# Optimization experiments

Hardware: AMD Instinct MI355X
Metric: run time of the kernel (lower is better)

Reference implementation:

```python
import jax, jax.numpy as jnp
import numpy as np

H = 56; W = 56; WS = 7; NW = WS * WS  # 49 tokens per window
HEADS = 8; DIM = 256; HIDDEN = 4 * DIM
SHIFT = NW // 2  # gilbert shift = 24 (shift_size > 0)
SCALE = (DIM // HEADS) ** -0.5
EPS = 1e-5


def _sgn(v):
    return -1 if v < 0 else 1 if v > 0 else 0


def _generate2d(x, y, ax, ay, bx, by, result):
    w = abs(ax + ay); h = abs(bx + by)
    dax, day = _sgn(ax), _sgn(ay); dbx, dby = _sgn(bx), _sgn(by)
    if h == 1 or w == 1:
        if h == 1:
            for _ in range(w):
                result.append((x, y)); x, y = x + dax, y + day
        elif w == 1:
            for _ in range(h):
                result.append((x, y)); x, y = x + dbx, y + dby
        return
    ax2, ay2 = ax // 2, ay // 2; bx2, by2 = bx // 2, by // 2
    w2 = abs(ax2 + ay2); h2 = abs(bx2 + by2)
    if 2 * w > 3 * h:
        if w2 % 2 and w > 2:
            ax2, ay2 = ax2 + dax, ay2 + day
        _generate2d(x, y, ax2, ay2, bx, by, result)
        _generate2d(x + ax2, y + ay2, ax - ax2, ay - ay2, bx, by, result)
    else:
        if h2 % 2 and h > 2:
            bx2, by2 = bx2 + dbx, by2 + dby
        _generate2d(x, y, bx2, by2, ax2, ay2, result)
        _generate2d(x + bx2, y + by2, ax, ay, bx - bx2, by - by2, result)
        _generate2d(x + (ax - dax) + (bx2 - dbx), y + (ay - day) + (by2 - dby),
                    -bx2, -by2, -(ax - ax2), -(ay - ay2), result)


def _gilbert2d(width, height):
    result = []
    if width >= height:
        _generate2d(0, 0, width, 0, 0, height, result)
    else:
        _generate2d(0, 0, 0, height, width, 0, result)
    return result


def _make_rel_index():
    # reverse_map[idx] = (y, x) for gilbert position idx
    path = _gilbert2d(W, H)
    rev = np.zeros((H * W, 2), dtype=np.int64)
    for i, (px, py) in enumerate(path[:H * W]):
        rev[i, 0] = py; rev[i, 1] = px
    pos = np.roll(rev, SHIFT, axis=0)  # shifted block: roll positions by ws^2//2
    n_windows = (H * W) // NW
    pos = pos[:n_windows * NW].reshape(n_windows, NW, 2)
    dh = pos[:, :, 0][:, :, None] - pos[:, :, 0][:, None, :] + (H - 1)
    dw = pos[:, :, 1][:, :, None] - pos[:, :, 1][:, None, :] + (W - 1)
    return (dh * (2 * W - 1) + dw).astype(np.int32)  # (nW, 49, 49)


def setup_inputs() -> dict:
    key = jax.random.key(0)
    ks = jax.random.split(key, 8)
    B, L, C = 32, H * W, DIM
    return {
        "x": jax.random.normal(ks[0], (B, L, C), jnp.float32),
        "qkv_w": jax.random.normal(ks[1], (C, 3 * C), jnp.float32) * 0.02,
        "qkv_b": jnp.zeros((3 * C,), jnp.float32),
        "proj_w": jax.random.normal(ks[2], (C, C), jnp.float32) * 0.02,
        "proj_b": jnp.zeros((C,), jnp.float32),
        "bias_table": jax.random.normal(ks[3], ((2 * H - 1) * (2 * W - 1), HEADS), jnp.float32) * 0.02,
        "norm1_w": jnp.ones((C,), jnp.float32),
        "norm1_b": jnp.zeros((C,), jnp.float32),
        "norm2_w": jnp.ones((C,), jnp.float32),
        "norm2_b": jnp.zeros((C,), jnp.float32),
        "fc1_w": jax.random.normal(ks[4], (C, HIDDEN), jnp.float32) * 0.02,
        "fc1_b": jnp.zeros((HIDDEN,), jnp.float32),
        "fc2_w": jax.random.normal(ks[5], (HIDDEN, C), jnp.float32) * 0.02,
        "fc2_b": jnp.zeros((C,), jnp.float32),
        "rel_index": jnp.asarray(_make_rel_index()),
    }


def _layernorm(x, w, b):
    mu = jnp.mean(x, axis=-1, keepdims=True)
    var = jnp.mean(jnp.square(x - mu), axis=-1, keepdims=True)
    return (x - mu) * jax.lax.rsqrt(var + EPS) * w + b


def reference(x, qkv_w, qkv_b, proj_w, proj_b, bias_table,
              norm1_w, norm1_b, norm2_w, norm2_b,
              fc1_w, fc1_b, fc2_w, fc2_b, rel_index):
    B, L, C = x.shape
    n_win = L // NW
    hd = C // HEADS

    shortcut = x
    h = _layernorm(x, norm1_w, norm1_b)
    # gilbert forward shift along the curve, then window partition
    h = jnp.roll(h, SHIFT, axis=1)
    hw = h.reshape(B * n_win, NW, C)

    qkv = (hw @ qkv_w + qkv_b).reshape(B * n_win, NW, 3, HEADS, hd)
    qkv = jnp.transpose(qkv, (2, 0, 3, 1, 4))  # (3, B*nW, heads, N, hd)
    q, k, v = qkv[0] * SCALE, qkv[1], qkv[2]

    attn = jnp.einsum('bhnd,bhmd->bhnm', q, k)  # (B*nW, heads, 49, 49)
    bias = jnp.transpose(bias_table[rel_index], (0, 3, 1, 2))  # (nW, heads, 49, 49)
    attn = attn.reshape(B, n_win, HEADS, NW, NW) + bias[None]
    attn = jax.nn.softmax(attn, axis=-1).reshape(B * n_win, HEADS, NW, NW)

    out = jnp.einsum('bhnm,bhmd->bhnd', attn, v)
    out = jnp.transpose(out, (0, 2, 1, 3)).reshape(B * n_win, NW, C)
    out = out @ proj_w + proj_b

    # window merge + gilbert reverse shift
    out = out.reshape(B, L, C)
    out = jnp.roll(out, -SHIFT, axis=1)

    x = shortcut + out
    h2 = _layernorm(x, norm2_w, norm2_b)
    h2 = jax.nn.gelu(h2 @ fc1_w + fc1_b, approximate=False) @ fc2_w + fc2_b
    return x + h2
```

## Files before the change

kernel.cpp:

```cpp
#include <hip/hip_runtime.h>
#include <math.h>

typedef unsigned short u16;
typedef __attribute__((ext_vector_type(8))) short bfrag;
typedef __attribute__((ext_vector_type(4))) float f32x4;
typedef __attribute__((ext_vector_type(4))) unsigned short us4;

#define B_SZ 32
#define L_SZ 3136
#define C_SZ 256
#define NHEADS 8
#define HID_SZ 1024
#define NW 49
#define NWIN 64
#define SHIFT 24
#define M_SZ (B_SZ * L_SZ)
#define SCALEF 0.17677669529663687f

__device__ __forceinline__ float bf2f(u16 u) {
  union { unsigned int i; float f; } v; v.i = ((unsigned)u) << 16; return v.f;
}
__device__ __forceinline__ u16 f2bf(float f) {
  union { unsigned int i; float f; } v; v.f = f;
  return (u16)((v.i + 0x7fffu + ((v.i >> 16) & 1u)) >> 16);
}
__device__ __forceinline__ void gload_lds16(const u16* g, u16* l) {
  __builtin_amdgcn_global_load_lds(
      (const __attribute__((address_space(1))) unsigned int*)g,
      (__attribute__((address_space(3))) unsigned int*)l, 16, 0, 0);
}

__global__ void transpose_kernel(const float* __restrict__ in, u16* __restrict__ out,
                                 int K, int N) {
  const int idx = blockIdx.x * 256 + threadIdx.x;
  if (idx >= K * N) return;
  const int n = idx / K;
  const int k = idx - n * K;
  out[idx] = f2bf(in[(size_t)k * N + n]);
}

__global__ void bias_kernel(const float* __restrict__ tab, const int* __restrict__ rel,
                            float* __restrict__ bm) {
  const int idx = blockIdx.x * 256 + threadIdx.x;
  const int tot = NWIN * NHEADS * NW * NW;
  if (idx >= tot) return;
  const int w = idx / (NHEADS * NW * NW);
  const int r = idx - w * (NHEADS * NW * NW);
  const int h = r / (NW * NW);
  const int ij = r - h * (NW * NW);
  bm[idx] = tab[(size_t)rel[w * NW * NW + ij] * NHEADS + h];
}

__global__ __launch_bounds__(256) void ln1_kernel(
    const float* __restrict__ x, const float* __restrict__ w,
    const float* __restrict__ b, u16* __restrict__ out) {
  const int wv = threadIdx.x >> 6;
  const int lane = threadIdx.x & 63;
  const int row0 = blockIdx.x * 16 + wv * 4;
  float4 u[4];
#pragma unroll
  for (int r = 0; r < 4; ++r)
    u[r] = *((const float4*)x + (size_t)(row0 + r) * 64 + lane);
  float s[4], sq[4];
#pragma unroll
  for (int r = 0; r < 4; ++r) {
    s[r]  = u[r].x + u[r].y + u[r].z + u[r].w;
    sq[r] = u[r].x * u[r].x + u[r].y * u[r].y + u[r].z * u[r].z + u[r].w * u[r].w;
  }
#pragma unroll
  for (int d = 1; d < 64; d <<= 1)
#pragma unroll
    for (int r = 0; r < 4; ++r) {
      s[r] += __shfl_xor(s[r], d); sq[r] += __shfl_xor(sq[r], d);
    }
  float wv4[4], bv4[4];
#pragma unroll
  for (int j = 0; j < 4; ++j) { wv4[j] = w[lane * 4 + j]; bv4[j] = b[lane * 4 + j]; }
#pragma unroll
  for (int r = 0; r < 4; ++r) {
    const int row = row0 + r;
    const float mu = s[r] * (1.0f / C_SZ);
    const float rs = rsqrtf(sq[r] * (1.0f / C_SZ) - mu * mu + 1e-5f);
    const int bb = row / L_SZ;
    int l2 = row - bb * L_SZ + SHIFT;
    if (l2 >= L_SZ) l2 -= L_SZ;
    const float vv[4] = {u[r].x, u[r].y, u[r].z, u[r].w};
    us4 ov;
#pragma unroll
    for (int j = 0; j < 4; ++j) ov[j] = f2bf((vv[j] - mu) * rs * wv4[j] + bv4[j]);
    *(us4*)(out + ((size_t)bb * L_SZ + l2) * C_SZ + lane * 4) = ov;
  }
}

__global__ __launch_bounds__(256) void ln2_kernel(
    const u16* __restrict__ x, const float* __restrict__ w,
    const float* __restrict__ b, u16* __restrict__ out) {
  const int wv = threadIdx.x >> 6;
  const int lane = threadIdx.x & 63;
  const int row0 = blockIdx.x * 16 + wv * 4;
  us4 u[4];
#pragma unroll
  for (int r = 0; r < 4; ++r)
    u[r] = *(const us4*)(x + (size_t)(row0 + r) * C_SZ + lane * 4);
  float v[4][4], s[4], sq[4];
#pragma unroll
  for (int r = 0; r < 4; ++r) {
    s[r] = 0.f; sq[r] = 0.f;
#pragma unroll
    for (int j = 0; j < 4; ++j) {
      v[r][j] = bf2f(u[r][j]); s[r] += v[r][j]; sq[r] += v[r][j] * v[r][j];
    }
  }
#pragma unroll
  for (int d = 1; d < 64; d <<= 1)
#pragma unroll
    for (int r = 0; r < 4; ++r) {
      s[r] += __shfl_xor(s[r], d); sq[r] += __shfl_xor(sq[r], d);
    }
  float wv4[4], bv4[4];
#pragma unroll
  for (int j = 0; j < 4; ++j) { wv4[j] = w[lane * 4 + j]; bv4[j] = b[lane * 4 + j]; }
#pragma unroll
  for (int r = 0; r < 4; ++r) {
    const float mu = s[r] * (1.0f / C_SZ);
    const float rs = rsqrtf(sq[r] * (1.0f / C_SZ) - mu * mu + 1e-5f);
    us4 ov;
#pragma unroll
    for (int j = 0; j < 4; ++j) ov[j] = f2bf((v[r][j] - mu) * rs * wv4[j] + bv4[j]);
    *(us4*)(out + (size_t)(row0 + r) * C_SZ + lane * 4) = ov;
  }
}

#define BM 128
#define BN 128
#define BKT 64

template <int MODE>
__global__ __launch_bounds__(256, 2) void gemm_kernel(
    const u16* __restrict__ A, const u16* __restrict__ Bt,
    const float* __restrict__ bias, int N, int K, void* __restrict__ Cout,
    const float* __restrict__ resx, u16* __restrict__ vt,
    const u16* __restrict__ resb2) {
  __shared__ u16 Als[BM * BKT];
  __shared__ u16 Bls[BN * BKT];
  const int tid = threadIdx.x;
  const int lane = tid & 63;
  const int lr = lane & 15;
  const int lg = lane >> 4;
  const int m0 = blockIdx.y * BM;
  const int n0 = blockIdx.x * BN;
  const int wid = tid >> 6;
  const int wm = (wid >> 1) * 64;
  const int wn = (wid & 1) * 64;

  const int grow = lane >> 3;
  const int gch = (lane & 7) ^ grow;

  const f32x4 fzero = {0.f, 0.f, 0.f, 0.f};
  f32x4 acc[4][4];
#pragma unroll
  for (int i = 0; i < 4; ++i)
#pragma unroll
    for (int j = 0; j < 4; ++j) acc[i][j] = fzero;

  const u16* Agl = A + (size_t)m0 * K + gch * 8;
  const u16* Bgl = Bt + (size_t)n0 * K + gch * 8;

  for (int k0 = 0; k0 < K; k0 += BKT) {
#pragma unroll
    for (int g = 0; g < 4; ++g) {
      const int rbase = wid * 32 + g * 8;
      gload_lds16(Agl + (size_t)(rbase + grow) * K + k0, Als + rbase * 64);
      gload_lds16(Bgl + (size_t)(rbase + grow) * K + k0, Bls + rbase * 64);
    }
    __syncthreads();
#pragma unroll
    for (int s = 0; s < 2; ++s) {
      const int kg = s * 4 + lg;
      bfrag af[4], bfv[4];
#pragma unroll
      for (int m = 0; m < 4; ++m) {
        const int r = wm + m * 16 + lr;
        af[m] = *(const bfrag*)(Als + r * 64 + ((kg ^ (r & 7)) * 8));
      }
#pragma unroll
      for (int n = 0; n < 4; ++n) {
        const int r = wn + n * 16 + lr;
        bfv[n] = *(const bfrag*)(Bls + r * 64 + ((kg ^ (r & 7)) * 8));
      }
#pragma unroll
      for (int m = 0; m < 4; ++m)
#pragma unroll
        for (int n = 0; n < 4; ++n)
          acc[m][n] = __builtin_amdgcn_mfma_f32_16x16x32_bf16(af[m], bfv[n],
                                                              acc[m][n], 0, 0, 0);
    }
    __syncthreads();
  }

  float bv4[4];
#pragma unroll
  for (int n = 0; n < 4; ++n) bv4[n] = bias[n0 + wn + n * 16 + lr];

#pragma unroll
  for (int m = 0; m < 4; ++m) {
#pragma unroll
    for (int i = 0; i < 4; ++i) {
      const int row = m0 + wm + m * 16 + lg * 4 + i;
      if (MODE == 1) {
        const int bb = row / L_SZ;
        int l2 = row - bb * L_SZ - SHIFT;
        if (l2 < 0) l2 += L_SZ;
        const size_t orow = (size_t)bb * L_SZ + l2;
#pragma unroll
        for (int n = 0; n < 4; ++n) {
          const int col = n0 + wn + n * 16 + lr;
          ((u16*)Cout)[orow * N + col] =
              f2bf(resx[orow * N + col] + acc[m][n][i] + bv4[n]);
        }
      } else if (MODE == 2) {
#pragma unroll
        for (int n = 0; n < 4; ++n) {
          const int col = n0 + wn + n * 16 + lr;
          float v = acc[m][n][i] + bv4[n];
          v = 0.5f * v * (1.0f + erff(v * 0.70710678f));
          ((u16*)Cout)[(size_t)row * N + col] = f2bf(v);
        }
      } else if (MODE == 3) {
#pragma unroll
        for (int n = 0; n < 4; ++n) {
          const int col = n0 + wn + n * 16 + lr;
          ((float*)Cout)[(size_t)row * N + col] =
              acc[m][n][i] + bv4[n] + bf2f(resb2[(size_t)row * N + col]);
        }
      } else {
        if (n0 + wn < 512) {
#pragma unroll
          for (int n = 0; n < 4; ++n) {
            const int col = n0 + wn + n * 16 + lr;
            ((u16*)Cout)[(size_t)row * 512 + col] = f2bf(acc[m][n][i] + bv4[n]);
          }
        } else {
          const unsigned widx = (unsigned)row / 49u;
          const int kk = row - (int)widx * 49;
#pragma unroll
          for (int n = 0; n < 4; ++n) {
            const int col = n0 + wn + n * 16 + lr - 512;
            const int hh = col >> 5;
            const int d = col & 31;
            vt[(((size_t)widx * NHEADS + hh) * 32 + d) * 64 + kk] =
                f2bf(acc[m][n][i] + bv4[n]);
          }
        }
      }
    }
  }
}

__global__ __launch_bounds__(256) void attn_kernel(const u16* __restrict__ qk,
                                                   const u16* __restrict__ vt,
                                                   const float* __restrict__ bm,
                                                   u16* __restrict__ out) {
  __shared__ u16 Pls[4][64 * 72];
  const int widx = blockIdx.x >> 1;
  const int half = blockIdx.x & 1;
  const int w = widx & (NWIN - 1);
  const int wv = threadIdx.x >> 6;
  const int lane = threadIdx.x & 63;
  const int lr = lane & 15;
  const int lg = lane >> 4;
  const size_t base = (size_t)widx * NW;
  u16* P = Pls[wv];
  const f32x4 fzero = {0.f, 0.f, 0.f, 0.f};
  const int h = half * 4 + wv;

  bfrag qf[4], kf[4];
#pragma unroll
  for (int m = 0; m < 4; ++m) {
    int r = m * 16 + lr; if (r > NW - 1) r = NW - 1;
    qf[m] = *(const bfrag*)(qk + (base + r) * 512 + h * 32 + lg * 8);
    kf[m] = *(const bfrag*)(qk + (base + r) * 512 + 256 + h * 32 + lg * 8);
  }
  f32x4 s[4][4];
#pragma unroll
  for (int m = 0; m < 4; ++m)
#pragma unroll
    for (int n = 0; n < 4; ++n)
      s[m][n] = __builtin_amdgcn_mfma_f32_16x16x32_bf16(qf[m], kf[n], fzero, 0, 0, 0);

  const float* bh = bm + (size_t)(w * NHEADS + h) * (NW * NW);
#pragma unroll
  for (int m = 0; m < 4; ++m) {
#pragma unroll
    for (int i = 0; i < 4; ++i) {
      const int row = m * 16 + lg * 4 + i;
      const int brow = row > NW - 1 ? NW - 1 : row;
      float vals[4];
#pragma unroll
      for (int n = 0; n < 4; ++n) {
        const int c = n * 16 + lr;
        vals[n] = (c < NW) ? (s[m][n][i] * SCALEF + bh[brow * NW + c]) : -1e30f;
      }
      float mx = fmaxf(fmaxf(vals[0], vals[1]), fmaxf(vals[2], vals[3]));
#pragma unroll
      for (int d = 1; d < 16; d <<= 1) mx = fmaxf(mx, __shfl_xor(mx, d));
      float sum = 0.f;
#pragma unroll
      for (int n = 0; n < 4; ++n) { vals[n] = __expf(vals[n] - mx); sum += vals[n]; }
#pragma unroll
      for (int d = 1; d < 16; d <<= 1) sum += __shfl_xor(sum, d);
      const float inv = 1.0f / sum;
#pragma unroll
      for (int n = 0; n < 4; ++n)
        P[row * 72 + n * 16 + lr] = f2bf(vals[n] * inv);
    }
  }
  const u16* vth = vt + ((size_t)widx * NHEADS + h) * 32 * 64;
  f32x4 o[4][2];
#pragma unroll
  for (int m = 0; m < 4; ++m) { o[m][0] = fzero; o[m][1] = fzero; }
#pragma unroll
  for (int s2 = 0; s2 < 2; ++s2) {
    bfrag pf[4], vf[2];
#pragma unroll
    for (int m = 0; m < 4; ++m)
      pf[m] = *(const bfrag*)(P + (m * 16 + lr) * 72 + s2 * 32 + lg * 8);
#pragma unroll
    for (int n = 0; n < 2; ++n)
      vf[n] = *(const bfrag*)(vth + (size_t)(n * 16 + lr) * 64 + s2 * 32 + lg * 8);
#pragma unroll
    for (int m = 0; m < 4; ++m)
#pragma unroll
      for (int n = 0; n < 2; ++n)
        o[m][n] = __builtin_amdgcn_mfma_f32_16x16x32_bf16(pf[m], vf[n],
                                                          o[m][n], 0, 0, 0);
  }
#pragma unroll
  for (int m = 0; m < 4; ++m)
#pragma unroll
    for (int i = 0; i < 4; ++i) {
      const int row = m * 16 + lg * 4 + i;
      if (row < NW) {
#pragma unroll
        for (int n = 0; n < 2; ++n)
          out[(base + row) * C_SZ + h * 32 + n * 16 + lr] = f2bf(o[m][n][i]);
      }
    }
}

extern "C" void kernel_launch(void* const* d_in, const int* in_sizes, int n_in,
                              void* d_out, int out_size, void* d_ws, size_t ws_size,
                              hipStream_t stream) {
  (void)in_sizes; (void)n_in; (void)out_size;
  const float* x     = (const float*)d_in[0];
  const float* qkvw  = (const float*)d_in[1];
  const float* qkvb  = (const float*)d_in[2];
  const float* projw = (const float*)d_in[3];
  const float* projb = (const float*)d_in[4];
  const float* btab  = (const float*)d_in[5];
  const float* n1w   = (const float*)d_in[6];
  const float* n1b   = (const float*)d_in[7];
  const float* n2w   = (const float*)d_in[8];
  const float* n2b   = (const float*)d_in[9];
  const float* fc1w  = (const float*)d_in[10];
  const float* fc1b  = (const float*)d_in[11];
  const float* fc2w  = (const float*)d_in[12];
  const float* fc2b  = (const float*)d_in[13];
  const int* rel     = (const int*)d_in[14];

  char* ws = (char*)d_ws;
  size_t off = 0;
  auto alloc = [&](size_t bytes) -> char* {
    char* p = ws + off; off += (bytes + 255) & ~(size_t)255; return p;
  };
  u16* qkvwT   = (u16*)alloc((size_t)768 * 256 * 2);
  u16* projwT  = (u16*)alloc((size_t)256 * 256 * 2);
  u16* fc1wT   = (u16*)alloc((size_t)1024 * 256 * 2);
  u16* fc2wT   = (u16*)alloc((size_t)256 * 1024 * 2);
  float* biasm = (float*)alloc((size_t)NWIN * NHEADS * NW * NW * 4);
  u16* bufh    = (u16*)alloc((size_t)M_SZ * C_SZ * 2);
  u16* x2b     = (u16*)alloc((size_t)M_SZ * C_SZ * 2);

  char* tail = ws + off;
  u16* qkbuf = (u16*)tail;
  const size_t qk_bytes = (size_t)M_SZ * 512 * 2;
  u16* vtbuf = (u16*)(tail + qk_bytes);
  const size_t tail_attn = qk_bytes + (size_t)B_SZ * NWIN * NHEADS * 32 * 64 * 2;
  u16* scratch2 = (u16*)tail;
  const size_t full_scr = (size_t)M_SZ * HID_SZ * 2;
  const size_t tail_need1 = full_scr > tail_attn ? full_scr : tail_attn;
  const int nch = (ws_size >= off + tail_need1) ? 1 : 4;
  const int mch = M_SZ / nch;

  transpose_kernel<<<(256 * 768 + 255) / 256, 256, 0, stream>>>(qkvw, qkvwT, 256, 768);
  transpose_kernel<<<(256 * 256 + 255) / 256, 256, 0, stream>>>(projw, projwT, 256, 256);
  transpose_kernel<<<(256 * 1024 + 255) / 256, 256, 0, stream>>>(fc1w, fc1wT, 256, 1024);
  transpose_kernel<<<(1024 * 256 + 255) / 256, 256, 0, stream>>>(fc2w, fc2wT, 1024, 256);
  bias_kernel<<<(NWIN * NHEADS * NW * NW + 255) / 256, 256, 0, stream>>>(btab, rel, biasm);

  ln1_kernel<<<M_SZ / 16, 256, 0, stream>>>(x, n1w, n1b, bufh);

  gemm_kernel<0><<<dim3(768 / BN, M_SZ / BM), 256, 0, stream>>>(
      bufh, qkvwT, qkvb, 768, 256, qkbuf, nullptr, vtbuf, nullptr);

  attn_kernel<<<B_SZ * NWIN * 2, 256, 0, stream>>>(qkbuf, vtbuf, biasm, bufh);

  gemm_kernel<1><<<dim3(256 / BN, M_SZ / BM), 256, 0, stream>>>(
      bufh, projwT, projb, 256, 256, x2b, x, nullptr, nullptr);

  for (int q = 0; q < nch; ++q) {
    const size_t roff = (size_t)q * mch;
    ln2_kernel<<<mch / 16, 256, 0, stream>>>(x2b + roff * C_SZ, n2w, n2b,
                                             bufh + roff * C_SZ);
    gemm_kernel<2><<<dim3(HID_SZ / BN, mch / BM), 256, 0, stream>>>(
        bufh + roff * C_SZ, fc1wT, fc1b, 1024, 256, scratch2, nullptr, nullptr, nullptr);
    gemm_kernel<3><<<dim3(256 / BN, mch / BM), 256, 0, stream>>>(
        scratch2, fc2wT, fc2b, 256, 1024, (float*)d_out + roff * C_SZ,
        nullptr, nullptr, x2b + roff * C_SZ);
  }
}
```

Before: 513.1 us.

## Write QKV row-major and transpose V in LDS; XCD-aware block remap for GEMMs

The QKV GEMM epilogue now writes plain row-major QKV instead of scattering V into a transposed per-window buffer. The attention kernel stages each head's V slice into swizzled LDS with async global-to-LDS loads and gathers transposed fragments element by element. All GEMMs switch to a 1D grid whose block index is remapped across the 8 XCDs so that neighbouring tiles share an L2. This removes the strided scattered V stores and shrinks workspace needs, but adds scalar LDS reads in attention.

```diff
diff --git a/kernel.cpp b/kernel.cpp
--- a/kernel.cpp
+++ b/kernel.cpp
@@ -139,16 +139,21 @@
 __global__ __launch_bounds__(256, 2) void gemm_kernel(
     const u16* __restrict__ A, const u16* __restrict__ Bt,
     const float* __restrict__ bias, int N, int K, void* __restrict__ Cout,
-    const float* __restrict__ resx, u16* __restrict__ vt,
-    const u16* __restrict__ resb2) {
+    const float* __restrict__ resx, const u16* __restrict__ resb2) {
   __shared__ u16 Als[BM * BKT];
   __shared__ u16 Bls[BN * BKT];
+  const int nbx = N / BN;
+  const int per = gridDim.x >> 3;
+  const int lin = (blockIdx.x & 7) * per + (blockIdx.x >> 3);
+  const int by = lin / nbx;
+  const int bx = lin - by * nbx;
+  const int m0 = by * BM;
+  const int n0 = bx * BN;
+
   const int tid = threadIdx.x;
   const int lane = tid & 63;
   const int lr = lane & 15;
   const int lg = lane >> 4;
-  const int m0 = blockIdx.y * BM;
-  const int n0 = blockIdx.x * BN;
   const int wid = tid >> 6;
   const int wm = (wid >> 1) * 64;
   const int wn = (wid & 1) * 64;
@@ -234,34 +239,21 @@
               acc[m][n][i] + bv4[n] + bf2f(resb2[(size_t)row * N + col]);
         }
       } else {
-        if (n0 + wn < 512) {
-#pragma unroll
-          for (int n = 0; n < 4; ++n) {
-            const int col = n0 + wn + n * 16 + lr;
-            ((u16*)Cout)[(size_t)row * 512 + col] = f2bf(acc[m][n][i] + bv4[n]);
-          }
-        } else {
-          const unsigned widx = (unsigned)row / 49u;
-          const int kk = row - (int)widx * 49;
-#pragma unroll
-          for (int n = 0; n < 4; ++n) {
-            const int col = n0 + wn + n * 16 + lr - 512;
-            const int hh = col >> 5;
-            const int d = col & 31;
-            vt[(((size_t)widx * NHEADS + hh) * 32 + d) * 64 + kk] =
-                f2bf(acc[m][n][i] + bv4[n]);
-          }
+#pragma unroll
+        for (int n = 0; n < 4; ++n) {
+          const int col = n0 + wn + n * 16 + lr;
+          ((u16*)Cout)[(size_t)row * N + col] = f2bf(acc[m][n][i] + bv4[n]);
         }
       }
     }
   }
 }
 
-__global__ __launch_bounds__(256) void attn_kernel(const u16* __restrict__ qk,
-                                                   const u16* __restrict__ vt,
+__global__ __launch_bounds__(256) void attn_kernel(const u16* __restrict__ qkv,
                                                    const float* __restrict__ bm,
                                                    u16* __restrict__ out) {
   __shared__ u16 Pls[4][64 * 72];
+  __shared__ u16 Vls[4][64 * 32];
   const int widx = blockIdx.x >> 1;
   const int half = blockIdx.x & 1;
   const int w = widx & (NWIN - 1);
@@ -271,15 +263,24 @@
   const int lg = lane >> 4;
   const size_t base = (size_t)widx * NW;
   u16* P = Pls[wv];
+  u16* Vl = Vls[wv];
   const f32x4 fzero = {0.f, 0.f, 0.f, 0.f};
   const int h = half * 4 + wv;
 
+#pragma unroll
+  for (int g = 0; g < 4; ++g) {
+    int row = g * 16 + (lane >> 2);
+    if (row > NW - 1) row = NW - 1;
+    const int sc = (lane & 3) ^ ((row ^ (row >> 2)) & 3);
+    gload_lds16(qkv + (base + row) * 768 + 512 + h * 32 + sc * 8, Vl + g * 512);
+  }
+
   bfrag qf[4], kf[4];
 #pragma unroll
   for (int m = 0; m < 4; ++m) {
     int r = m * 16 + lr; if (r > NW - 1) r = NW - 1;
-    qf[m] = *(const bfrag*)(qk + (base + r) * 512 + h * 32 + lg * 8);
-    kf[m] = *(const bfrag*)(qk + (base + r) * 512 + 256 + h * 32 + lg * 8);
+    qf[m] = *(const bfrag*)(qkv + (base + r) * 768 + h * 32 + lg * 8);
+    kf[m] = *(const bfrag*)(qkv + (base + r) * 768 + 256 + h * 32 + lg * 8);
   }
   f32x4 s[4][4];
 #pragma unroll
@@ -315,7 +316,7 @@
         P[row * 72 + n * 16 + lr] = f2bf(vals[n] * inv);
     }
   }
-  const u16* vth = vt + ((size_t)widx * NHEADS + h) * 32 * 64;
+  asm volatile("s_waitcnt vmcnt(0)" ::: "memory");
   f32x4 o[4][2];
 #pragma unroll
   for (int m = 0; m < 4; ++m) { o[m][0] = fzero; o[m][1] = fzero; }
@@ -326,8 +327,16 @@
     for (int m = 0; m < 4; ++m)
       pf[m] = *(const bfrag*)(P + (m * 16 + lr) * 72 + s2 * 32 + lg * 8);
 #pragma unroll
-    for (int n = 0; n < 2; ++n)
-      vf[n] = *(const bfrag*)(vth + (size_t)(n * 16 + lr) * 64 + s2 * 32 + lg * 8);
+    for (int n = 0; n < 2; ++n) {
+      const int d = n * 16 + lr;
+      const int cd = d >> 3;
+#pragma unroll
+      for (int i = 0; i < 8; ++i) {
+        const int kk = s2 * 32 + lg * 8 + i;
+        const int slot = cd ^ ((kk ^ (kk >> 2)) & 3);
+        vf[n][i] = *(const short*)(Vl + kk * 32 + slot * 8 + (d & 7));
+      }
+    }
 #pragma unroll
     for (int m = 0; m < 4; ++m)
 #pragma unroll
@@ -382,14 +391,10 @@
   u16* x2b     = (u16*)alloc((size_t)M_SZ * C_SZ * 2);
 
   char* tail = ws + off;
-  u16* qkbuf = (u16*)tail;
-  const size_t qk_bytes = (size_t)M_SZ * 512 * 2;
-  u16* vtbuf = (u16*)(tail + qk_bytes);
-  const size_t tail_attn = qk_bytes + (size_t)B_SZ * NWIN * NHEADS * 32 * 64 * 2;
+  u16* qkvbuf   = (u16*)tail;
   u16* scratch2 = (u16*)tail;
   const size_t full_scr = (size_t)M_SZ * HID_SZ * 2;
-  const size_t tail_need1 = full_scr > tail_attn ? full_scr : tail_attn;
-  const int nch = (ws_size >= off + tail_need1) ? 1 : 4;
+  const int nch = (ws_size >= off + full_scr) ? 1 : 4;
   const int mch = M_SZ / nch;
 
   transpose_kernel<<<(256 * 768 + 255) / 256, 256, 0, stream>>>(qkvw, qkvwT, 256, 768);
@@ -400,22 +405,22 @@
 
   ln1_kernel<<<M_SZ / 16, 256, 0, stream>>>(x, n1w, n1b, bufh);
 
-  gemm_kernel<0><<<dim3(768 / BN, M_SZ / BM), 256, 0, stream>>>(
-      bufh, qkvwT, qkvb, 768, 256, qkbuf, nullptr, vtbuf, nullptr);
-
-  attn_kernel<<<B_SZ * NWIN * 2, 256, 0, stream>>>(qkbuf, vtbuf, biasm, bufh);
-
-  gemm_kernel<1><<<dim3(256 / BN, M_SZ / BM), 256, 0, stream>>>(
-      bufh, projwT, projb, 256, 256, x2b, x, nullptr, nullptr);
+  gemm_kernel<0><<<(768 / BN) * (M_SZ / BM), 256, 0, stream>>>(
+      bufh, qkvwT, qkvb, 768, 256, qkvbuf, nullptr, nullptr);
+
+  attn_kernel<<<B_SZ * NWIN * 2, 256, 0, stream>>>(qkvbuf, biasm, bufh);
+
+  gemm_kernel<1><<<(256 / BN) * (M_SZ / BM), 256, 0, stream>>>(
+      bufh, projwT, projb, 256, 256, x2b, x, nullptr);
 
   for (int q = 0; q < nch; ++q) {
     const size_t roff = (size_t)q * mch;
     ln2_kernel<<<mch / 16, 256, 0, stream>>>(x2b + roff * C_SZ, n2w, n2b,
                                              bufh + roff * C_SZ);
-    gemm_kernel<2><<<dim3(HID_SZ / BN, mch / BM), 256, 0, stream>>>(
-        bufh + roff * C_SZ, fc1wT, fc1b, 1024, 256, scratch2, nullptr, nullptr, nullptr);
-    gemm_kernel<3><<<dim3(256 / BN, mch / BM), 256, 0, stream>>>(
+    gemm_kernel<2><<<(HID_SZ / BN) * (mch / BM), 256, 0, stream>>>(
+        bufh + roff * C_SZ, fc1wT, fc1b, 1024, 256, scratch2, nullptr, nullptr);
+    gemm_kernel<3><<<(256 / BN) * (mch / BM), 256, 0, stream>>>(
         scratch2, fc2wT, fc2b, 256, 1024, (float*)d_out + roff * C_SZ,
-        nullptr, nullptr, x2b + roff * C_SZ);
-  }
-}
+        nullptr, x2b + roff * C_SZ);
+  }
+}
```

Result: faster. 456.8 us (-11.0%).
